# Optimization experiments

Measured on AMD Instinct MI355X. Metric: run time of the kernel, lower is better.

Reference implementation:

```python
import jax, jax.numpy as jnp
import numpy as np

N = 512      # HiPPO state size
L = 65536    # sequence length
DT = 1e-3    # discretization step
UNROLL = 32  # scan unroll (source uses 128; 32 keeps CPU compile fast, same math)


def _make_hippo(n_state):
    # HiPPO-LegS continuous-time (A, B), as in make_hippo
    n = np.arange(n_state)
    P = np.sqrt(1 + 2 * n)
    A = P[:, None] * P[None, :]
    A = np.tril(A) - np.diag(n)
    B = np.sqrt(2 * n + 1.0)[:, None]
    return -A, B


def _discretize(A, B, step):
    # Bilinear (Tustin) discretization, as in discretize
    I = np.eye(A.shape[0])
    BL = np.linalg.inv(I - step / 2 * A)
    Ab = BL @ (I + step / 2 * A)
    Bb = (BL * step) @ B
    return Ab, Bb


def setup_inputs() -> dict:
    key = jax.random.key(0)
    A, B = _make_hippo(N)            # float64 numpy for stable inverse
    Ab, Bb = _discretize(A, B, DT)
    u = jax.random.normal(key, (L,), dtype=jnp.float32)
    return {
        "u": u,
        "Ab": jnp.asarray(Ab, dtype=jnp.float32),   # [N, N]
        "Bb": jnp.asarray(Bb, dtype=jnp.float32),   # [N, 1]
        "x0": jnp.zeros((N,), dtype=jnp.float32),   # last_x initial state
    }


def reference(u, Ab, Bb, x0):
    # Faithful HiPPO.encode: x_{k+1} = Ab @ x_k + Bb @ u_k, returning the
    # full state trajectory f of shape [L, N] (the scan's stacked outputs).
    b = Bb[:, 0]  # Bb @ u[k, None] == b * u_k

    def step(x, u_k):
        x1 = Ab @ x + b * u_k
        return x1, x1

    _, f = jax.lax.scan(step, x0, u, unroll=UNROLL)
    return f
```

## Files before the change

kernel.cpp:

```cpp
#include <hip/hip_runtime.h>
#include <cstdint>
#include <cstddef>


typedef _Float16 half_t;
typedef _Float16 f16x8 __attribute__((ext_vector_type(8)));
typedef float f32x4 __attribute__((ext_vector_type(4)));

static constexpr int KPAD = 544;
static constexpr size_t MSZ = (size_t)512 * 512;
static constexpr float INV2048 = 1.f / 2048.f;

__device__ inline void split1(float v, half_t& h, half_t& l) {
  h = (half_t)v;
  l = (half_t)((v - (float)h) * 2048.f);
}
__device__ inline void split1r(float v, half_t& h, half_t& l) {
  h = (half_t)v;
  l = (half_t)(v - (float)h);
}

template <int NKT, bool ATOM>
__device__ __forceinline__ void sq_body(
    const float* __restrict__ A, const float* __restrict__ B, float* __restrict__ C,
    int bx, int by, int k0off,
    half_t* __restrict__ Ash, half_t* __restrict__ Asl,
    half_t* __restrict__ Bsh, half_t* __restrict__ Bsl) {
  int m0 = bx * 64, n0 = by * 64;
  int tid = threadIdx.x, wave = tid >> 6, lane = tid & 63;
  int wm = (wave & 1) * 32, wn = (wave >> 1) * 32;
  f32x4 acc[2][2], accc[2][2];
#pragma unroll
  for (int i = 0; i < 2; ++i)
#pragma unroll
    for (int j = 0; j < 2; ++j) {
      acc[i][j] = (f32x4){0.f, 0.f, 0.f, 0.f};
      accc[i][j] = (f32x4){0.f, 0.f, 0.f, 0.f};
    }
  int rb = tid >> 6, mm = tid & 15, kseg = (tid >> 4) & 3;
  const float* ar = A + (size_t)(m0 + rb * 16 + mm) * 512 + k0off + kseg * 8;
  const float* bc = B + (size_t)(k0off + kseg * 8) * 512 + n0 + rb * 16 + mm;
  float4 a0 = *(const float4*)ar, a1 = *(const float4*)(ar + 4);
  float bv[8];
#pragma unroll
  for (int j = 0; j < 8; ++j) bv[j] = bc[(size_t)j * 512];
#pragma unroll
  for (int kt = 0; kt < NKT; ++kt) {
    {
      float aa[8] = {a0.x, a0.y, a0.z, a0.w, a1.x, a1.y, a1.z, a1.w};
      f16x8 hv, lv;
#pragma unroll
      for (int j = 0; j < 8; ++j) { half_t h, l; split1(aa[j], h, l); hv[j] = h; lv[j] = l; }
      *(f16x8*)(Ash + tid * 8) = hv;
      *(f16x8*)(Asl + tid * 8) = lv;
#pragma unroll
      for (int j = 0; j < 8; ++j) { half_t h, l; split1(bv[j], h, l); hv[j] = h; lv[j] = l; }
      *(f16x8*)(Bsh + tid * 8) = hv;
      *(f16x8*)(Bsl + tid * 8) = lv;
    }
    __syncthreads();
    if (kt < NKT - 1) {
      a0 = *(const float4*)(ar + (kt + 1) * 32);
      a1 = *(const float4*)(ar + (kt + 1) * 32 + 4);
#pragma unroll
      for (int j = 0; j < 8; ++j) bv[j] = bc[(size_t)((kt + 1) * 32 + j) * 512];
    }
    f16x8 afh[2], afl[2], bfh[2], bfl[2];
#pragma unroll
    for (int i = 0; i < 2; ++i) {
      int ra = (wm >> 4) + i, rbn = (wn >> 4) + i;
      afh[i] = *(const f16x8*)(Ash + ra * 512 + lane * 8);
      afl[i] = *(const f16x8*)(Asl + ra * 512 + lane * 8);
      bfh[i] = *(const f16x8*)(Bsh + rbn * 512 + lane * 8);
      bfl[i] = *(const f16x8*)(Bsl + rbn * 512 + lane * 8);
    }
#pragma unroll
    for (int i = 0; i < 2; ++i)
#pragma unroll
      for (int j = 0; j < 2; ++j) {
        acc[i][j] = __builtin_amdgcn_mfma_f32_16x16x32_f16(afh[i], bfh[j], acc[i][j], 0, 0, 0);
        accc[i][j] = __builtin_amdgcn_mfma_f32_16x16x32_f16(afh[i], bfl[j], accc[i][j], 0, 0, 0);
        accc[i][j] = __builtin_amdgcn_mfma_f32_16x16x32_f16(afl[i], bfh[j], accc[i][j], 0, 0, 0);
      }
    __syncthreads();
  }
  int ml = lane & 15, quad = lane >> 4;
  for (int i = 0; i < 2; ++i)
    for (int j = 0; j < 2; ++j)
      for (int rr = 0; rr < 4; ++rr) {
        int gm = m0 + wm + i * 16 + quad * 4 + rr;
        int gn = n0 + wn + j * 16 + ml;
        float v = acc[i][j][rr] + accc[i][j][rr] * INV2048;
        if (ATOM) atomicAdd(&C[(size_t)gm * 512 + gn], v);
        else C[(size_t)gm * 512 + gn] = v;
      }
}

__device__ __forceinline__ void sweep_body(
    const half_t* __restrict__ A, long ldA, const float* __restrict__ BT,
    const half_t* __restrict__ D, long ldD,
    half_t* __restrict__ Ch, half_t* __restrict__ Cl, long ldC,
    int rScale, int rOff, int doCopy, int M, int bx, int by,
    half_t* __restrict__ Ash, half_t* __restrict__ Bsh, half_t* __restrict__ Bsl) {
  int m0 = bx * 64, n0 = by * 64;
  int tid = threadIdx.x, wave = tid >> 6, lane = tid & 63;
  int wm = (wave & 1) * 32, wn = (wave >> 1) * 32;
  f32x4 acc[2][2], accc[2][2];
#pragma unroll
  for (int i = 0; i < 2; ++i)
#pragma unroll
    for (int j = 0; j < 2; ++j) {
      acc[i][j] = (f32x4){0.f, 0.f, 0.f, 0.f};
      accc[i][j] = (f32x4){0.f, 0.f, 0.f, 0.f};
    }
  int rb = tid >> 6, mm = tid & 15, kseg = (tid >> 4) & 3;
  int arow = m0 + rb * 16 + mm;
  const half_t* ap = A + (size_t)arow * ldA + kseg * 8;
  const float* bp = BT + (size_t)(n0 + rb * 16 + mm) * 512 + kseg * 8;
  f16x8 av = (f16x8){0, 0, 0, 0, 0, 0, 0, 0};
  if (arow < M) av = *(const f16x8*)ap;
  float4 bv0 = *(const float4*)bp;
  float4 bv1 = *(const float4*)(bp + 4);
#pragma unroll
  for (int kt = 0; kt < 16; ++kt) {
    int k0 = kt * 32;
    *(f16x8*)(Ash + tid * 8) = av;
    if (doCopy && k0 >= n0 && k0 < n0 + 64 && arow < M) {
      size_t co = (size_t)rScale * arow * ldC + k0 + kseg * 8;
      *(f16x8*)(Ch + co) = av;
      if (Cl) *(f16x8*)(Cl + co) = (f16x8){0, 0, 0, 0, 0, 0, 0, 0};
    }
    {
      float bb[8] = {bv0.x, bv0.y, bv0.z, bv0.w, bv1.x, bv1.y, bv1.z, bv1.w};
      f16x8 hv, lv;
#pragma unroll
      for (int j = 0; j < 8; ++j) { half_t h, l; split1(bb[j], h, l); hv[j] = h; lv[j] = l; }
      *(f16x8*)(Bsh + tid * 8) = hv;
      *(f16x8*)(Bsl + tid * 8) = lv;
    }
    __syncthreads();
    if (kt < 15) {
      if (arow < M) av = *(const f16x8*)(ap + (kt + 1) * 32);
      bv0 = *(const float4*)(bp + (kt + 1) * 32);
      bv1 = *(const float4*)(bp + (kt + 1) * 32 + 4);
    }
    f16x8 af[2], bfh[2], bfl[2];
#pragma unroll
    for (int i = 0; i < 2; ++i) {
      af[i] = *(const f16x8*)(Ash + ((wm >> 4) + i) * 512 + lane * 8);
      bfh[i] = *(const f16x8*)(Bsh + ((wn >> 4) + i) * 512 + lane * 8);
      bfl[i] = *(const f16x8*)(Bsl + ((wn >> 4) + i) * 512 + lane * 8);
    }
#pragma unroll
    for (int i = 0; i < 2; ++i)
#pragma unroll
      for (int j = 0; j < 2; ++j) {
        acc[i][j] = __builtin_amdgcn_mfma_f32_16x16x32_f16(af[i], bfh[j], acc[i][j], 0, 0, 0);
        accc[i][j] = __builtin_amdgcn_mfma_f32_16x16x32_f16(af[i], bfl[j], accc[i][j], 0, 0, 0);
      }
    __syncthreads();
  }
  int ml = lane & 15, quad = lane >> 4;
  for (int i = 0; i < 2; ++i)
    for (int j = 0; j < 2; ++j)
      for (int rr = 0; rr < 4; ++rr) {
        int gm = m0 + wm + i * 16 + quad * 4 + rr;
        int gn = n0 + wn + j * 16 + ml;
        if (gm >= M) continue;
        float v = acc[i][j][rr] + accc[i][j][rr] * INV2048;
        if (D) v += (float)D[(size_t)gm * ldD + gn];
        size_t co = ((size_t)gm * rScale + rOff) * ldC + gn;
        if (Cl) { half_t h, l; split1r(v, h, l); Ch[co] = h; Cl[co] = l; }
        else Ch[co] = (half_t)v;
      }
}

__device__ __forceinline__ size_t zoff_f(int l) {
  return ((size_t)1 << 22) - ((size_t)1 << (22 - l));
}


__global__ void init_kernel(float4* __restrict__ zp, const float* __restrict__ Ab,
                            float* __restrict__ V0, const float* __restrict__ x0,
                            half_t* __restrict__ xh) {
  int bid = blockIdx.x, tid = threadIdx.x;
  if (bid < 6656) {
    zp[bid * 256 + tid] = make_float4(0.f, 0.f, 0.f, 0.f);
  } else if (bid < 7680) {
    int i = (bid - 6656) * 256 + tid;
    V0[i] = Ab[i];
  } else {
    xh[tid] = (half_t)x0[tid];
    xh[tid + 256] = (half_t)x0[tid + 256];
  }
}

__global__ void kbuild_kernel(const float* __restrict__ V, const float* __restrict__ b,
                              float* __restrict__ K) {
  int gw = blockIdx.x * 4 + (threadIdx.x >> 6);
  int lane = threadIdx.x & 63;
  int t = gw >> 9, n = gw & 511;
  if (t == 0) { if (lane == 0) K[n] = b[n]; return; }
  const float* row = V + (size_t)(t - 1) * MSZ + (size_t)n * 512;
  float acc = 0.f;
#pragma unroll
  for (int m = 0; m < 512; m += 64) acc += row[m + lane] * b[m + lane];
#pragma unroll
  for (int s = 32; s; s >>= 1) acc += __shfl_down(acc, s, 64);
  if (lane == 0) K[t * 512 + n] = acc;
}

__global__ void wcat_fill_kernel(const float* __restrict__ V, const float* __restrict__ K,
                                 half_t* __restrict__ Wh, half_t* __restrict__ Wl) {
  int un = blockIdx.x * 256 + threadIdx.x;
  if (un >= 8192 * 68) return;
  int row = un / 68, kb = un - row * 68;
  int i = row >> 9, n = row & 511;
  f16x8 hv, lv;
  if (kb < 64) {
    const float* vp = V + (size_t)i * MSZ + (size_t)n * 512 + kb * 8;
    float4 v0 = *(const float4*)vp, v1 = *(const float4*)(vp + 4);
    float vv[8] = {v0.x, v0.y, v0.z, v0.w, v1.x, v1.y, v1.z, v1.w};
#pragma unroll
    for (int j = 0; j < 8; ++j) { half_t h, l; split1r(vv[j], h, l); hv[j] = h; lv[j] = l; }
  } else {
#pragma unroll
    for (int j = 0; j < 8; ++j) {
      int k = kb * 8 + j;
      float v = 0.f;
      if (k < 528) { int jj = k - 512; if (jj <= i) v = K[(i - jj) * 512 + n]; }
      half_t h, l; split1r(v, h, l); hv[j] = h; lv[j] = l;
    }
  }
  size_t o = (size_t)row * KPAD + kb * 8;
  *(f16x8*)(Wh + o) = hv;
  *(f16x8*)(Wl + o) = lv;
}

__global__ void leaf_kernel(const float* __restrict__ u, const float* __restrict__ K,
                            half_t* __restrict__ Z) {
  __shared__ float us[16];
  int c = blockIdx.x, n = threadIdx.x;
  if (n < 16) us[n] = u[c * 16 + n];
  __syncthreads();
  float acc = 0.f;
#pragma unroll
  for (int j = 0; j < 16; ++j) acc += K[(15 - j) * 512 + n] * us[j];
  Z[(size_t)c * 512 + n] = (half_t)acc;
}

__global__ __launch_bounds__(256)
void gemm_nn512(const float* __restrict__ A, long sA,
                const float* __restrict__ B, long sB,
                float* __restrict__ C, long sC) {
  __shared__ __align__(16) half_t s0[64 * 32], s1[64 * 32], s2[64 * 32], s3[64 * 32];
  int bz = blockIdx.z, bb = bz >> 2, sl = bz & 3;
  sq_body<4, true>(A + (size_t)bb * sA, B + (size_t)bb * sB, C + (size_t)bb * sC,
                   blockIdx.x, blockIdx.y, sl * 128, s0, s1, s2, s3);
}

__global__ __launch_bounds__(256)
void fused_up(const float* __restrict__ T, float* __restrict__ Tout,
              const half_t* __restrict__ Zin, half_t* __restrict__ Zout, int M) {
  __shared__ __align__(16) half_t s0[64 * 32], s1[64 * 32], s2[64 * 32], s3[64 * 32];
  int bid = blockIdx.x;
  if (bid < 256) {
    sq_body<4, true>(T, T, Tout, bid & 7, (bid >> 3) & 7, (bid >> 6) * 128, s0, s1, s2, s3);
  } else {
    int b = bid - 256;
    sweep_body(Zin, 1024L, T, Zin + 512, 1024L, Zout, (half_t*)0, 512L,
               1, 0, 0, M, b >> 3, b & 7, s0, s1, s2);
  }
}

__global__ __launch_bounds__(256)
void prep_kernel(const float* __restrict__ Vp, const float* __restrict__ Sp,
                 const half_t* __restrict__ Zh, half_t* __restrict__ YZp,
                 float* __restrict__ P10, float* __restrict__ S1c) {
  __shared__ __align__(16) half_t s0[64 * 32], s1[64 * 32], s2[64 * 32], s3[64 * 32];
  int bid = blockIdx.x, tid = threadIdx.x;
  if (bid < 64) {
    sq_body<16, false>(Sp + (size_t)9 * MSZ, Sp + (size_t)10 * MSZ, P10,
                       bid & 7, bid >> 3, 0, s0, s1, s2, s3);
    return;
  }
  int yb = bid - 64;
  const int yzr[6] = {0, 1, 5, 21, 85, 341};
#pragma unroll
  for (int t = 0; t < 6; ++t) {
    int l = 10 - 2 * t;
    int M0 = 1 << (2 * t);
    int nb = ((M0 + 63) >> 6) * 8;
    if (yb < nb) {
      const float* Sl = (l == 0) ? Vp + 15 * MSZ : Sp + (size_t)(l - 1) * MSZ;
      sweep_body(Zh + zoff_f(l + 1), 1024L, Sl,
                 Zh + zoff_f(l) + 1024, 2048L,
                 YZp + (size_t)yzr[t] * 512, (half_t*)0, 512L,
                 1, 0, 0, M0, yb >> 3, yb & 7, s0, s1, s2);
      return;
    }
    yb -= nb;
  }
  ((float4*)S1c)[(size_t)yb * 256 + tid] = ((const float4*)Sp)[(size_t)yb * 256 + tid];
}

__global__ __launch_bounds__(256)
void down_pair(const half_t* __restrict__ Xin, int M0,
               const float* __restrict__ Sl, const float* __restrict__ Sl1,
               const float* __restrict__ Pl,
               const half_t* __restrict__ Zl, const half_t* __restrict__ Zl1,
               const half_t* __restrict__ YZ,
               half_t* __restrict__ Ch, half_t* __restrict__ Cl, long ldC,
               const float* __restrict__ Pna, const float* __restrict__ Pnb,
               float* __restrict__ Pnout, const float* __restrict__ uu) {
  __shared__ __align__(16) half_t s0[64 * 32], s1[64 * 32], s2[64 * 32], s3[64 * 32];
  int bid = blockIdx.x, tid = threadIdx.x;
  int nrole = ((M0 + 63) >> 6) * 8;
  if (bid < 3 * nrole) {
    int r = bid / nrole, b = bid - r * nrole;
    const float* BT = (r == 0) ? Sl : (r == 1) ? Sl1 : Pl;
    const half_t* D = (r == 0) ? Zl : (r == 1) ? Zl1 : YZ;
    long ldD = (r == 0) ? 2048L : (r == 1) ? 1024L : 512L;
    sweep_body(Xin, 512L, BT, D, ldD, Ch, Cl, ldC,
               4, r + 1, (r == 0) ? 1 : 0, M0, b >> 3, b & 7, s0, s1, s2);
    return;
  }
  int rest = bid - 3 * nrole;
  if (Pnout) {
    sq_body<16, false>(Pna, Pnb, Pnout, rest & 7, rest >> 3, 0, s0, s1, s2, s3);
    return;
  }
  int idx = rest * 256 + tid;
  int c = idx >> 5, j = idx & 31;
  float v = (j < 16) ? uu[c * 16 + j] : 0.f;
  size_t o = (size_t)c * KPAD + 512 + j;
  half_t h, l; split1r(v, h, l);
  Ch[o] = h; Cl[o] = l;
}

__device__ inline void load_lds16(const half_t* g, half_t* l) {
  __builtin_amdgcn_global_load_lds(
      (const __attribute__((address_space(1))) uint32_t*)g,
      (__attribute__((address_space(3))) uint32_t*)l, 16, 0, 0);
}

__global__ __launch_bounds__(512, 2)
void gemm_main(const half_t* __restrict__ Ah, const half_t* __restrict__ Al,
               const half_t* __restrict__ Bh, const half_t* __restrict__ Bl,
               float* __restrict__ C) {
  __shared__ __align__(16) half_t sm[2 * 4 * 8192];
  int bid = blockIdx.x;
  int xcd = bid & 7, loc = bid >> 3;
  int mt = (xcd & 1) * 8 + (loc >> 3);
  int nt = (xcd >> 1) * 8 + (loc & 7);
  int m0 = mt * 256, n0 = nt * 256;
  int tid = threadIdx.x, wave = tid >> 6, lane = tid & 63;
  int wm = (wave & 1) * 128, wn = (wave >> 1) * 64;
  int mm = lane & 15, kseg = lane >> 4;
  f32x4 acc[8][4];
#pragma unroll
  for (int f = 0; f < 8; ++f)
#pragma unroll
    for (int g = 0; g < 4; ++g) acc[f][g] = (f32x4){0.f, 0.f, 0.f, 0.f};

  const size_t ga0 = (size_t)(m0 + wave * 16 + mm) * KPAD + kseg * 8;
  const size_t gb0 = (size_t)(n0 + wave * 16 + mm) * KPAD + kseg * 8;
  const size_t qstep = (size_t)128 * KPAD;

  auto stage = [&](int nb, int kt, int q) {
    size_t go = (size_t)kt * 32 + (size_t)q * qstep;
    half_t* d = sm + (size_t)nb * 32768 + (size_t)(wave + 8 * q) * 512;
    load_lds16(Ah + ga0 + go, d);
    load_lds16(Al + ga0 + go, d + 8192);
    load_lds16(Bh + gb0 + go, d + 16384);
    load_lds16(Bl + gb0 + go, d + 24576);
  };

  stage(0, 0, 0);
  stage(0, 0, 1);
  asm volatile("s_waitcnt vmcnt(0)" ::: "memory");
  __builtin_amdgcn_s_barrier();

  const int lread = lane * 8;
  const int arow = (wm >> 4);
  const int brow = (wn >> 4);
  for (int kt = 0; kt < 17; ++kt) {
    const int cur = kt & 1;
    const half_t* SA_h = sm + cur * 32768;
    const half_t* SA_l = SA_h + 8192;
    const half_t* SB_h = SA_h + 16384;
    const half_t* SB_l = SA_h + 24576;
    const bool pre = kt < 16;
    f16x8 ah[4], al[4], bh0[2], bl0[2], bh1[2], bl1[2];

#pragma unroll
    for (int i = 0; i < 4; ++i) {
      ah[i] = *(const f16x8*)(SA_h + (arow + i) * 512 + lread);
      al[i] = *(const f16x8*)(SA_l + (arow + i) * 512 + lread);
    }
#pragma unroll
    for (int j = 0; j < 2; ++j) {
      bh0[j] = *(const f16x8*)(SB_h + (brow + j) * 512 + lread);
      bl0[j] = *(const f16x8*)(SB_l + (brow + j) * 512 + lread);
    }
    if (pre) stage(cur ^ 1, kt + 1, 0);
    __builtin_amdgcn_s_barrier();
    asm volatile("s_waitcnt lgkmcnt(0)" ::: "memory");
    __builtin_amdgcn_sched_barrier(0);
    __builtin_amdgcn_s_setprio(1);
#pragma unroll
    for (int i = 0; i < 4; ++i)
#pragma unroll
      for (int j = 0; j < 2; ++j) {
        acc[i][j] = __builtin_amdgcn_mfma_f32_16x16x32_f16(ah[i], bh0[j], acc[i][j], 0, 0, 0);
        acc[i][j] = __builtin_amdgcn_mfma_f32_16x16x32_f16(ah[i], bl0[j], acc[i][j], 0, 0, 0);
        acc[i][j] = __builtin_amdgcn_mfma_f32_16x16x32_f16(al[i], bh0[j], acc[i][j], 0, 0, 0);
      }
    __builtin_amdgcn_s_setprio(0);
    __builtin_amdgcn_s_barrier();

#pragma unroll
    for (int j = 0; j < 2; ++j) {
      bh1[j] = *(const f16x8*)(SB_h + (brow + 2 + j) * 512 + lread);
      bl1[j] = *(const f16x8*)(SB_l + (brow + 2 + j) * 512 + lread);
    }
    if (pre) stage(cur ^ 1, kt + 1, 1);
    __builtin_amdgcn_s_barrier();
    asm volatile("s_waitcnt lgkmcnt(0)" ::: "memory");
    __builtin_amdgcn_sched_barrier(0);
    __builtin_amdgcn_s_setprio(1);
#pragma unroll
    for (int i = 0; i < 4; ++i)
#pragma unroll
      for (int j = 0; j < 2; ++j) {
        acc[i][2 + j] = __builtin_amdgcn_mfma_f32_16x16x32_f16(ah[i], bh1[j], acc[i][2 + j], 0, 0, 0);
        acc[i][2 + j] = __builtin_amdgcn_mfma_f32_16x16x32_f16(ah[i], bl1[j], acc[i][2 + j], 0, 0, 0);
        acc[i][2 + j] = __builtin_amdgcn_mfma_f32_16x16x32_f16(al[i], bh1[j], acc[i][2 + j], 0, 0, 0);
      }
    __builtin_amdgcn_s_setprio(0);
    __builtin_amdgcn_s_barrier();

#pragma unroll
    for (int i = 0; i < 4; ++i) {
      ah[i] = *(const f16x8*)(SA_h + (arow + 4 + i) * 512 + lread);
      al[i] = *(const f16x8*)(SA_l + (arow + 4 + i) * 512 + lread);
    }
    __builtin_amdgcn_s_barrier();
    asm volatile("s_waitcnt lgkmcnt(0)" ::: "memory");
    __builtin_amdgcn_sched_barrier(0);
    __builtin_amdgcn_s_setprio(1);
#pragma unroll
    for (int i = 0; i < 4; ++i)
#pragma unroll
      for (int j = 0; j < 2; ++j) {
        acc[4 + i][2 + j] = __builtin_amdgcn_mfma_f32_16x16x32_f16(ah[i], bh1[j], acc[4 + i][2 + j], 0, 0, 0);
        acc[4 + i][2 + j] = __builtin_amdgcn_mfma_f32_16x16x32_f16(ah[i], bl1[j], acc[4 + i][2 + j], 0, 0, 0);
        acc[4 + i][2 + j] = __builtin_amdgcn_mfma_f32_16x16x32_f16(al[i], bh1[j], acc[4 + i][2 + j], 0, 0, 0);
      }
#pragma unroll
    for (int i = 0; i < 4; ++i)
#pragma unroll
      for (int j = 0; j < 2; ++j) {
        acc[4 + i][j] = __builtin_amdgcn_mfma_f32_16x16x32_f16(ah[i], bh0[j], acc[4 + i][j], 0, 0, 0);
        acc[4 + i][j] = __builtin_amdgcn_mfma_f32_16x16x32_f16(ah[i], bl0[j], acc[4 + i][j], 0, 0, 0);
        acc[4 + i][j] = __builtin_amdgcn_mfma_f32_16x16x32_f16(al[i], bh0[j], acc[4 + i][j], 0, 0, 0);
      }
    __builtin_amdgcn_s_setprio(0);
    asm volatile("s_waitcnt vmcnt(0)" ::: "memory");
    __builtin_amdgcn_s_barrier();
  }

  int ml = lane & 15, quad = lane >> 4;
#pragma unroll
  for (int f = 0; f < 8; ++f)
#pragma unroll
    for (int g = 0; g < 4; ++g) {
      int gm = m0 + wm + f * 16 + quad * 4;
      int gn = n0 + wn + g * 16 + ml;
      float* o = C + (size_t)gm * 8192 + gn;
#pragma unroll
      for (int rr = 0; rr < 4; ++rr)
        o[(size_t)rr * 8192] = acc[f][g][rr];
    }
}


extern "C" void kernel_launch(void* const* d_in, const int* in_sizes, int n_in,
                              void* d_out, int out_size, void* d_ws, size_t ws_size,
                              hipStream_t stream) {
  (void)in_sizes; (void)n_in; (void)out_size; (void)ws_size;
  const float* u  = (const float*)d_in[0];
  const float* Ab = (const float*)d_in[1];
  const float* Bb = (const float*)d_in[2];
  const float* x0 = (const float*)d_in[3];
  float* out = (float*)d_out;

  char* base = (char*)d_ws;
  size_t off = 0;
  auto carve = [&](size_t bytes) -> char* {
    char* p = base + off;
    off = (off + bytes + 255) & ~(size_t)255;
    return p;
  };
  float*  Vp  = (float*)carve(16 * MSZ * 4);
  float*  Sp  = (float*)carve(11 * MSZ * 4);
  float*  Kb  = (float*)carve((size_t)16 * 512 * 4);
  half_t* Wh  = (half_t*)carve((size_t)8192 * KPAD * 2);
  half_t* Wl  = (half_t*)carve((size_t)8192 * KPAD * 2);
  half_t* x0h = (half_t*)carve(512 * 2);
  float*  Pp  = (float*)carve(3 * MSZ * 4);
  float*  Pb0 = Pp;
  float*  Pb1 = Pp + MSZ;
  float*  S1c = Pp + 2 * MSZ;

  size_t zoff[13]; zoff[0] = 0;
  for (int l = 0; l < 12; ++l) zoff[l + 1] = zoff[l] + (size_t)(4096 >> l) * 512;
  size_t xoff[13]; xoff[1] = 0;
  for (int l = 1; l < 12; ++l) xoff[l + 1] = xoff[l] + (size_t)(4096 >> l) * 512;
  half_t* Zh  = (half_t*)Vp;
  size_t xphOff = (zoff[12] * 2 + 255) & ~(size_t)255;
  half_t* Xph = (half_t*)((char*)Vp + xphOff);
  half_t* YZp = (half_t*)((char*)Vp + xphOff + ((xoff[12] * 2 + 255) & ~(size_t)255));
  half_t* Xch = (half_t*)Sp;
  half_t* Xcl = (half_t*)((char*)Sp + (((size_t)4096 * KPAD * 2 + 255) & ~(size_t)255));

  hipLaunchKernelGGL(init_kernel, dim3(7681), dim3(256), 0, stream,
                     (float4*)(Vp + MSZ), Ab, Vp, x0, x0h);

  for (int s = 1; s <= 8; s <<= 1) {
    hipLaunchKernelGGL(gemm_nn512, dim3(8, 8, 4 * s), dim3(256), 0, stream,
                       Vp, (long)MSZ,
                       Vp + (size_t)(s - 1) * MSZ, 0L,
                       Vp + (size_t)s * MSZ, (long)MSZ);
  }
  hipLaunchKernelGGL(kbuild_kernel, dim3(2048), dim3(256), 0, stream, Vp, Bb, Kb);
  hipLaunchKernelGGL(wcat_fill_kernel, dim3(2176), dim3(256), 0, stream, Vp, Kb, Wh, Wl);
  hipLaunchKernelGGL(leaf_kernel, dim3(4096), dim3(512), 0, stream, u, Kb, Zh);

  auto Smat = [&](int l) -> const float* {
    return (l == 0) ? (Vp + 15 * MSZ) : (Sp + (size_t)(l - 1) * MSZ);
  };

  for (int l = 1; l <= 11; ++l) {
    const float* T = Smat(l - 1);
    float* Tout = Sp + (size_t)(l - 1) * MSZ;
    int Mup = 1 << (12 - l);
    int nswp = ((Mup + 63) / 64) * 8;
    hipLaunchKernelGGL(fused_up, dim3(256 + nswp), dim3(256), 0, stream,
                       T, Tout, Zh + zoff[l - 1], Zh + zoff[l], Mup);
  }

  hipLaunchKernelGGL(prep_kernel, dim3(512), dim3(256), 0, stream,
                     Vp, Sp, Zh, YZp, Pb0, S1c);

  const int yzrow[6] = {0, 1, 5, 21, 85, 341};
  for (int i = 0; i < 6; ++i) {
    int l = 10 - 2 * i;
    int M0 = 1 << (2 * i);
    const float* Sl  = Smat(l);
    const float* Sl1 = (i == 5) ? S1c : Smat(l + 1);
    const float* Pl  = (i & 1) ? Pb1 : Pb0;
    const float* Pna = (i < 5) ? Smat(l - 2) : (const float*)0;
    const float* Pnb = (i < 5) ? Smat(l - 1) : (const float*)0;
    float* Pnout     = (i < 5) ? ((i & 1) ? Pb0 : Pb1) : (float*)0;
    const half_t* Xin = (i == 0) ? x0h : Xph + xoff[l + 2];
    half_t* Ch = (i == 5) ? Xch : Xph + xoff[l];
    half_t* Cl = (i == 5) ? Xcl : (half_t*)0;
    long ldC = (i == 5) ? (long)KPAD : 512L;
    const float* uu = (i == 5) ? u : (const float*)0;
    int nrole = ((M0 + 63) / 64) * 8;
    int grid = 3 * nrole + (i < 5 ? 64 : 0) + (i == 5 ? 512 : 0);
    hipLaunchKernelGGL(down_pair, dim3(grid), dim3(256), 0, stream,
                       Xin, M0, Sl, Sl1, Pl,
                       Zh + zoff[l], Zh + zoff[l + 1],
                       YZp + (size_t)yzrow[i] * 512,
                       Ch, Cl, ldC, Pna, Pnb, Pnout, uu);
  }

  hipLaunchKernelGGL(gemm_main, dim3(512), dim3(512), 0, stream, Xch, Xcl, Wh, Wl, out);
}
```

Before: 642.2 us.

## Halve gemm_main N-tile to 128 and use triple-buffered LDS prefetch

```diff
diff --git a/kernel.cpp b/kernel.cpp
--- a/kernel.cpp
+++ b/kernel.cpp
@@ -348,62 +348,60 @@
 void gemm_main(const half_t* __restrict__ Ah, const half_t* __restrict__ Al,
                const half_t* __restrict__ Bh, const half_t* __restrict__ Bl,
                float* __restrict__ C) {
-  __shared__ __align__(16) half_t sm[2 * 4 * 8192];
+  __shared__ __align__(16) half_t sm[3 * 24576];
   int bid = blockIdx.x;
   int xcd = bid & 7, loc = bid >> 3;
-  int mt = (xcd & 1) * 8 + (loc >> 3);
-  int nt = (xcd >> 1) * 8 + (loc & 7);
-  int m0 = mt * 256, n0 = nt * 256;
+  int mt = (xcd & 1) * 8 + (loc >> 4);
+  int nt = (xcd >> 1) * 16 + (loc & 15);
+  int m0 = mt * 256, n0 = nt * 128;
   int tid = threadIdx.x, wave = tid >> 6, lane = tid & 63;
-  int wm = (wave & 1) * 128, wn = (wave >> 1) * 64;
+  int wm = (wave & 1) * 128, wn = (wave >> 1) * 32;
   int mm = lane & 15, kseg = lane >> 4;
-  f32x4 acc[8][4];
+  f32x4 acc[8][2];
 #pragma unroll
   for (int f = 0; f < 8; ++f)
 #pragma unroll
-    for (int g = 0; g < 4; ++g) acc[f][g] = (f32x4){0.f, 0.f, 0.f, 0.f};
+    for (int g = 0; g < 2; ++g) acc[f][g] = (f32x4){0.f, 0.f, 0.f, 0.f};
 
   const size_t ga0 = (size_t)(m0 + wave * 16 + mm) * KPAD + kseg * 8;
   const size_t gb0 = (size_t)(n0 + wave * 16 + mm) * KPAD + kseg * 8;
   const size_t qstep = (size_t)128 * KPAD;
 
-  auto stage = [&](int nb, int kt, int q) {
-    size_t go = (size_t)kt * 32 + (size_t)q * qstep;
-    half_t* d = sm + (size_t)nb * 32768 + (size_t)(wave + 8 * q) * 512;
-    load_lds16(Ah + ga0 + go, d);
-    load_lds16(Al + ga0 + go, d + 8192);
-    load_lds16(Bh + gb0 + go, d + 16384);
-    load_lds16(Bl + gb0 + go, d + 24576);
+  auto stage = [&](int buf, int kt) {
+    size_t go = (size_t)kt * 32;
+    half_t* base = sm + (size_t)buf * 24576;
+    load_lds16(Ah + ga0 + go, base + wave * 512);
+    load_lds16(Al + ga0 + go, base + 8192 + wave * 512);
+    load_lds16(Ah + ga0 + qstep + go, base + (wave + 8) * 512);
+    load_lds16(Al + ga0 + qstep + go, base + 8192 + (wave + 8) * 512);
+    load_lds16(Bh + gb0 + go, base + 16384 + wave * 512);
+    load_lds16(Bl + gb0 + go, base + 20480 + wave * 512);
   };
 
-  stage(0, 0, 0);
-  stage(0, 0, 1);
-  asm volatile("s_waitcnt vmcnt(0)" ::: "memory");
+  stage(0, 0);
+  stage(1, 1);
+  asm volatile("s_waitcnt vmcnt(6)" ::: "memory");
   __builtin_amdgcn_s_barrier();
 
   const int lread = lane * 8;
-  const int arow = (wm >> 4);
-  const int brow = (wn >> 4);
+  const int arg = (wave & 1) * 8;
+  const int brg = (wave >> 1) * 2;
+  int cur = 0;
   for (int kt = 0; kt < 17; ++kt) {
-    const int cur = kt & 1;
-    const half_t* SA_h = sm + cur * 32768;
-    const half_t* SA_l = SA_h + 8192;
-    const half_t* SB_h = SA_h + 16384;
-    const half_t* SB_l = SA_h + 24576;
-    const bool pre = kt < 16;
-    f16x8 ah[4], al[4], bh0[2], bl0[2], bh1[2], bl1[2];
+    const half_t* base = sm + cur * 24576;
+    f16x8 ah[4], al[4], bh[2], bl[2];
 
 #pragma unroll
     for (int i = 0; i < 4; ++i) {
-      ah[i] = *(const f16x8*)(SA_h + (arow + i) * 512 + lread);
-      al[i] = *(const f16x8*)(SA_l + (arow + i) * 512 + lread);
+      ah[i] = *(const f16x8*)(base + (arg + i) * 512 + lread);
+      al[i] = *(const f16x8*)(base + 8192 + (arg + i) * 512 + lread);
     }
 #pragma unroll
     for (int j = 0; j < 2; ++j) {
-      bh0[j] = *(const f16x8*)(SB_h + (brow + j) * 512 + lread);
-      bl0[j] = *(const f16x8*)(SB_l + (brow + j) * 512 + lread);
-    }
-    if (pre) stage(cur ^ 1, kt + 1, 0);
+      bh[j] = *(const f16x8*)(base + 16384 + (brg + j) * 512 + lread);
+      bl[j] = *(const f16x8*)(base + 20480 + (brg + j) * 512 + lread);
+    }
+    if (kt < 15) stage(cur ? cur - 1 : 2, kt + 2);
     __builtin_amdgcn_s_barrier();
     asm volatile("s_waitcnt lgkmcnt(0)" ::: "memory");
     __builtin_amdgcn_sched_barrier(0);
@@ -412,19 +410,18 @@
     for (int i = 0; i < 4; ++i)
 #pragma unroll
       for (int j = 0; j < 2; ++j) {
-        acc[i][j] = __builtin_amdgcn_mfma_f32_16x16x32_f16(ah[i], bh0[j], acc[i][j], 0, 0, 0);
-        acc[i][j] = __builtin_amdgcn_mfma_f32_16x16x32_f16(ah[i], bl0[j], acc[i][j], 0, 0, 0);
-        acc[i][j] = __builtin_amdgcn_mfma_f32_16x16x32_f16(al[i], bh0[j], acc[i][j], 0, 0, 0);
+        acc[i][j] = __builtin_amdgcn_mfma_f32_16x16x32_f16(ah[i], bh[j], acc[i][j], 0, 0, 0);
+        acc[i][j] = __builtin_amdgcn_mfma_f32_16x16x32_f16(ah[i], bl[j], acc[i][j], 0, 0, 0);
+        acc[i][j] = __builtin_amdgcn_mfma_f32_16x16x32_f16(al[i], bh[j], acc[i][j], 0, 0, 0);
       }
     __builtin_amdgcn_s_setprio(0);
     __builtin_amdgcn_s_barrier();
 
 #pragma unroll
-    for (int j = 0; j < 2; ++j) {
-      bh1[j] = *(const f16x8*)(SB_h + (brow + 2 + j) * 512 + lread);
-      bl1[j] = *(const f16x8*)(SB_l + (brow + 2 + j) * 512 + lread);
-    }
-    if (pre) stage(cur ^ 1, kt + 1, 1);
+    for (int i = 0; i < 4; ++i) {
+      ah[i] = *(const f16x8*)(base + (arg + 4 + i) * 512 + lread);
+      al[i] = *(const f16x8*)(base + 8192 + (arg + 4 + i) * 512 + lread);
+    }
     __builtin_amdgcn_s_barrier();
     asm volatile("s_waitcnt lgkmcnt(0)" ::: "memory");
     __builtin_amdgcn_sched_barrier(0);
@@ -433,48 +430,22 @@
     for (int i = 0; i < 4; ++i)
 #pragma unroll
       for (int j = 0; j < 2; ++j) {
-        acc[i][2 + j] = __builtin_amdgcn_mfma_f32_16x16x32_f16(ah[i], bh1[j], acc[i][2 + j], 0, 0, 0);
-        acc[i][2 + j] = __builtin_amdgcn_mfma_f32_16x16x32_f16(ah[i], bl1[j], acc[i][2 + j], 0, 0, 0);
-        acc[i][2 + j] = __builtin_amdgcn_mfma_f32_16x16x32_f16(al[i], bh1[j], acc[i][2 + j], 0, 0, 0);
+        acc[4 + i][j] = __builtin_amdgcn_mfma_f32_16x16x32_f16(ah[i], bh[j], acc[4 + i][j], 0, 0, 0);
+        acc[4 + i][j] = __builtin_amdgcn_mfma_f32_16x16x32_f16(ah[i], bl[j], acc[4 + i][j], 0, 0, 0);
+        acc[4 + i][j] = __builtin_amdgcn_mfma_f32_16x16x32_f16(al[i], bh[j], acc[4 + i][j], 0, 0, 0);
       }
     __builtin_amdgcn_s_setprio(0);
+    if (kt < 15) asm volatile("s_waitcnt vmcnt(6)" ::: "memory");
+    else asm volatile("s_waitcnt vmcnt(0)" ::: "memory");
     __builtin_amdgcn_s_barrier();
-
-#pragma unroll
-    for (int i = 0; i < 4; ++i) {
-      ah[i] = *(const f16x8*)(SA_h + (arow + 4 + i) * 512 + lread);
-      al[i] = *(const f16x8*)(SA_l + (arow + 4 + i) * 512 + lread);
-    }
-    __builtin_amdgcn_s_barrier();
-    asm volatile("s_waitcnt lgkmcnt(0)" ::: "memory");
-    __builtin_amdgcn_sched_barrier(0);
-    __builtin_amdgcn_s_setprio(1);
-#pragma unroll
-    for (int i = 0; i < 4; ++i)
-#pragma unroll
-      for (int j = 0; j < 2; ++j) {
-        acc[4 + i][2 + j] = __builtin_amdgcn_mfma_f32_16x16x32_f16(ah[i], bh1[j], acc[4 + i][2 + j], 0, 0, 0);
-        acc[4 + i][2 + j] = __builtin_amdgcn_mfma_f32_16x16x32_f16(ah[i], bl1[j], acc[4 + i][2 + j], 0, 0, 0);
-        acc[4 + i][2 + j] = __builtin_amdgcn_mfma_f32_16x16x32_f16(al[i], bh1[j], acc[4 + i][2 + j], 0, 0, 0);
-      }
-#pragma unroll
-    for (int i = 0; i < 4; ++i)
-#pragma unroll
-      for (int j = 0; j < 2; ++j) {
-        acc[4 + i][j] = __builtin_amdgcn_mfma_f32_16x16x32_f16(ah[i], bh0[j], acc[4 + i][j], 0, 0, 0);
-        acc[4 + i][j] = __builtin_amdgcn_mfma_f32_16x16x32_f16(ah[i], bl0[j], acc[4 + i][j], 0, 0, 0);
-        acc[4 + i][j] = __builtin_amdgcn_mfma_f32_16x16x32_f16(al[i], bh0[j], acc[4 + i][j], 0, 0, 0);
-      }
-    __builtin_amdgcn_s_setprio(0);
-    asm volatile("s_waitcnt vmcnt(0)" ::: "memory");
-    __builtin_amdgcn_s_barrier();
+    cur = (cur == 2) ? 0 : cur + 1;
   }
 
   int ml = lane & 15, quad = lane >> 4;
 #pragma unroll
   for (int f = 0; f < 8; ++f)
 #pragma unroll
-    for (int g = 0; g < 4; ++g) {
+    for (int g = 0; g < 2; ++g) {
       int gm = m0 + wm + f * 16 + quad * 4;
       int gn = n0 + wn + g * 16 + ml;
       float* o = C + (size_t)gm * 8192 + gn;
@@ -577,5 +548,5 @@
                        Ch, Cl, ldC, Pna, Pnb, Pnout, uu);
   }
 
-  hipLaunchKernelGGL(gemm_main, dim3(512), dim3(512), 0, stream, Xch, Xcl, Wh, Wl, out);
-}
+  hipLaunchKernelGGL(gemm_main, dim3(1024), dim3(512), 0, stream, Xch, Xcl, Wh, Wl, out);
+}
```

Result: no change. 645.0 us (+0.4%).
